# Kernel tuning notes

Measured on AMD Instinct MI355X. Metric: run time of the kernel, lower is better.

The kernel has to match this reference:

```python
import jax, jax.numpy as jnp
import numpy as np

D_MODEL = 1024
N_HEADS = 16
HEAD_DIM = D_MODEL // N_HEADS


def setup_inputs() -> dict:
    key = jax.random.key(0)
    ks = jax.random.split(key, 5)
    B, T = 4, 4096
    x = jax.random.normal(ks[0], (B, T, D_MODEL), dtype=jnp.float32)
    s = 1.0 / np.sqrt(D_MODEL)
    Wqkv = jax.random.normal(ks[1], (D_MODEL, 3 * D_MODEL), dtype=jnp.float32) * s
    bqkv = jnp.zeros((3 * D_MODEL,), dtype=jnp.float32)
    Wout = jax.random.normal(ks[2], (D_MODEL, D_MODEL), dtype=jnp.float32) * s
    bout = jnp.zeros((D_MODEL,), dtype=jnp.float32)
    return {"x": x, "Wqkv": Wqkv, "bqkv": bqkv, "Wout": Wout, "bout": bout}


def _feature_map(x):
    # elu(x) + 1  (strictly positive feature map)
    return jax.nn.elu(x) + 1.0


def reference(x, Wqkv, bqkv, Wout, bout):
    B, T, C = x.shape
    H, D = N_HEADS, HEAD_DIM
    qkv = x @ Wqkv + bqkv                      # [B,T,3C]
    qkv = qkv.reshape(B, T, 3, H, D)
    qkv = jnp.transpose(qkv, (2, 0, 3, 1, 4))  # [3,B,H,T,D]
    q, k, v = qkv[0], qkv[1], qkv[2]
    scale = D ** 0.25
    q_m = _feature_map(q / scale)
    k_m = _feature_map(k / scale)
    kv = jnp.einsum('bhtd,bhtm->bhdm', k_m, v)     # [B,H,D,D]
    out = jnp.einsum('bhtd,bhdm->bhtm', q_m, kv)   # [B,H,T,D]
    z = q_m.sum(axis=-1, keepdims=True)            # note: sum over feature dim (as in source)
    out = out / (z + 1e-6)
    out = jnp.transpose(out, (0, 2, 1, 3)).reshape(B, T, C)
    return out @ Wout + bout
```

## Files before the change

kernel.cpp:

```cpp
#include <hip/hip_runtime.h>
#include <hip/hip_bf16.h>
#include <math.h>

#define B_ 4
#define T_ 4096
#define H_ 16
#define D_ 64
#define C_ 1024
#define BT_ (B_*T_)

using short8  = __attribute__((ext_vector_type(8))) short;
using floatx4 = __attribute__((ext_vector_type(4))) float;

__device__ __forceinline__ float feature_map(float x) {
    return x > 0.0f ? x + 1.0f : __expf(x);
}
__device__ __forceinline__ unsigned short f2bf(float x) {
    union { __hip_bfloat16 b; unsigned short u; } c;
    c.b = __float2bfloat16(x);
    return c.u;
}
__device__ __forceinline__ float bf2f(unsigned short u) {
    union { unsigned int u; float f; } c;
    c.u = (unsigned)u << 16;
    return c.f;
}
__device__ __forceinline__ void async16(const void* g, void* l) {
    __builtin_amdgcn_global_load_lds(
        (const __attribute__((address_space(1))) void*)g,
        (__attribute__((address_space(3))) void*)l, 16, 0, 0);
}

__global__ __launch_bounds__(256)
void convert_x_kernel(const float4* __restrict__ x, ushort* __restrict__ xb)
{
    const size_t i = (size_t)blockIdx.x * 256 + threadIdx.x;
    const float4 v = x[i];
    *reinterpret_cast<ushort4*>(&xb[i * 4]) =
        make_ushort4(f2bf(v.x), f2bf(v.y), f2bf(v.z), f2bf(v.w));
}

__global__ __launch_bounds__(256)
void transpose_bf16_kernel(const float* __restrict__ W, ushort* __restrict__ WT,
                           int K, int N)
{
    __shared__ float t[32][33];
    const int n0 = blockIdx.x * 32, k0 = blockIdx.y * 32;
    const int r = threadIdx.x >> 5, c = threadIdx.x & 31;
    #pragma unroll
    for (int i = 0; i < 4; i++)
        t[r + 8 * i][c] = W[(size_t)(k0 + r + 8 * i) * N + n0 + c];
    __syncthreads();
    #pragma unroll
    for (int i = 0; i < 4; i++)
        WT[(size_t)(n0 + r + 8 * i) * K + k0 + c] = f2bf(t[c][r + 8 * i]);
}

__global__ __launch_bounds__(256)
void qkv_mfma_kernel(const ushort* __restrict__ xb, const ushort* __restrict__ WqkvT,
                     const float* __restrict__ bqkv,
                     ushort* __restrict__ qm, ushort* __restrict__ kmT,
                     ushort* __restrict__ vT)
{
    __shared__ __align__(16) unsigned char smem[16384];
    ushort* As = (ushort*)smem;
    ushort* Bs = (ushort*)(smem + 8192);

    const int tid = threadIdx.x;
    const int w = tid >> 6, l = tid & 63;
    const int wm = w >> 1, wn = w & 1;
    const int lr = l & 15, quad = l >> 4;
    const int lk8 = quad * 8;
    const int nBase = blockIdx.x * 128;
    const int mBase = blockIdx.y * 128;

    const int srow = w * 32 + (l >> 2);
    const int scol = (l & 3) * 8;
    const ushort* gA = xb + (size_t)(mBase + srow) * C_ + scol;
    const ushort* gB = WqkvT + (size_t)(nBase + srow) * C_ + scol;
    void* ldsA = (void*)(smem + w * 2048);
    void* ldsB = (void*)(smem + 8192 + w * 2048);

    floatx4 acc[4][4];
    #pragma unroll
    for (int i = 0; i < 4; i++)
        #pragma unroll
        for (int j = 0; j < 4; j++) acc[i][j] = (floatx4)0.0f;

    for (int k0 = 0; k0 < C_; k0 += 32) {
        __syncthreads();
        async16(gA + k0, ldsA);
        async16(gA + 16 * C_ + k0, (void*)((char*)ldsA + 1024));
        async16(gB + k0, ldsB);
        async16(gB + 16 * C_ + k0, (void*)((char*)ldsB + 1024));
        __syncthreads();

        short8 af[4], bf[4];
        #pragma unroll
        for (int mt = 0; mt < 4; mt++)
            af[mt] = *(const short8*)&As[(wm * 64 + mt * 16 + lr) * 32 + lk8];
        #pragma unroll
        for (int nt = 0; nt < 4; nt++)
            bf[nt] = *(const short8*)&Bs[(wn * 64 + nt * 16 + lr) * 32 + lk8];
        #pragma unroll
        for (int mt = 0; mt < 4; mt++)
            #pragma unroll
            for (int nt = 0; nt < 4; nt++)
                acc[mt][nt] = __builtin_amdgcn_mfma_f32_16x16x32_bf16(
                    af[mt], bf[nt], acc[mt][nt], 0, 0, 0);
    }

    const float inv_scale = 0.35355339059327373f;
    const int seg = nBase >> 10;

    if (seg == 0) {
        #pragma unroll
        for (int nt = 0; nt < 4; nt++) {
            const int c = nBase + wn * 64 + nt * 16 + lr;
            const float bv = bqkv[c];
            #pragma unroll
            for (int mt = 0; mt < 4; mt++)
                #pragma unroll
                for (int i = 0; i < 4; i++) {
                    const int t = mBase + wm * 64 + mt * 16 + quad * 4 + i;
                    qm[(size_t)t * C_ + c] =
                        f2bf(feature_map((acc[mt][nt][i] + bv) * inv_scale));
                }
        }
    } else {
        ushort* dstT = (seg == 1) ? kmT : vT;
        #pragma unroll
        for (int nt = 0; nt < 4; nt++) {
            const int cfull = nBase + wn * 64 + nt * 16 + lr;
            const int c = cfull - (seg << 10);
            const float bv = bqkv[cfull];
            #pragma unroll
            for (int mt = 0; mt < 4; mt++) {
                float v0 = acc[mt][nt][0] + bv, v1 = acc[mt][nt][1] + bv;
                float v2 = acc[mt][nt][2] + bv, v3 = acc[mt][nt][3] + bv;
                if (seg == 1) {
                    v0 = feature_map(v0 * inv_scale); v1 = feature_map(v1 * inv_scale);
                    v2 = feature_map(v2 * inv_scale); v3 = feature_map(v3 * inv_scale);
                }
                const int t = mBase + wm * 64 + mt * 16 + quad * 4;
                *(ushort4*)&dstT[(size_t)c * BT_ + t] =
                    make_ushort4(f2bf(v0), f2bf(v1), f2bf(v2), f2bf(v3));
            }
        }
    }
}

__global__ __launch_bounds__(256)
void kv_accum_kernel(const ushort* __restrict__ kmT, const ushort* __restrict__ vT,
                     float* __restrict__ kv)
{
    const int tid = threadIdx.x;
    const int w = tid >> 6, l = tid & 63;
    const int wm = w >> 1, wn = w & 1;
    const int lr = l & 15, quad = l >> 4;
    const int bh = blockIdx.y;
    const int b = bh >> 4, h = bh & 15;
    const size_t t0 = (size_t)b * T_ + (size_t)blockIdx.x * 512;

    const ushort* Ar = kmT + (size_t)(h * 64 + wm * 32 + lr) * BT_ + t0 + quad * 8;
    const ushort* Br = vT  + (size_t)(h * 64 + wn * 32 + lr) * BT_ + t0 + quad * 8;

    floatx4 acc[2][2];
    #pragma unroll
    for (int i = 0; i < 2; i++)
        #pragma unroll
        for (int j = 0; j < 2; j++) acc[i][j] = (floatx4)0.0f;

    #pragma unroll 4
    for (int tt = 0; tt < 512; tt += 32) {
        const short8 af0 = *(const short8*)&Ar[tt];
        const short8 af1 = *(const short8*)&Ar[(size_t)16 * BT_ + tt];
        const short8 bf0 = *(const short8*)&Br[tt];
        const short8 bf1 = *(const short8*)&Br[(size_t)16 * BT_ + tt];
        acc[0][0] = __builtin_amdgcn_mfma_f32_16x16x32_bf16(af0, bf0, acc[0][0], 0, 0, 0);
        acc[0][1] = __builtin_amdgcn_mfma_f32_16x16x32_bf16(af0, bf1, acc[0][1], 0, 0, 0);
        acc[1][0] = __builtin_amdgcn_mfma_f32_16x16x32_bf16(af1, bf0, acc[1][0], 0, 0, 0);
        acc[1][1] = __builtin_amdgcn_mfma_f32_16x16x32_bf16(af1, bf1, acc[1][1], 0, 0, 0);
    }

    float* kvb = kv + (size_t)bh * (D_ * D_);
    #pragma unroll
    for (int i = 0; i < 2; i++)
        #pragma unroll
        for (int j = 0; j < 2; j++)
            #pragma unroll
            for (int r = 0; r < 4; r++) {
                const int d = wm * 32 + i * 16 + quad * 4 + r;
                const int m = wn * 32 + j * 16 + lr;
                atomicAdd(&kvb[d * 64 + m], acc[i][j][r]);
            }
}

__global__ __launch_bounds__(256)
void pv_kernel(const ushort* __restrict__ qm, const float* __restrict__ kv,
               ushort* __restrict__ attn)
{
    __shared__ ushort kvs[64 * 72];
    const int tid = threadIdx.x;
    const int w = tid >> 6, l = tid & 63;
    const int lr = l & 15, quad = l >> 4;
    const int h = blockIdx.x;
    const int tBase = blockIdx.y * 256;
    const int b = tBase >> 12;

    const float* kvg = kv + ((size_t)b * H_ + h) * (D_ * D_);
    #pragma unroll
    for (int e = 0; e < 4; e++) {
        const int flat = (e * 256 + tid) * 4;
        const float4 vv = *(const float4*)&kvg[flat];
        const int d = flat >> 6, m = flat & 63;
        kvs[(m + 0) * 72 + d] = f2bf(vv.x);
        kvs[(m + 1) * 72 + d] = f2bf(vv.y);
        kvs[(m + 2) * 72 + d] = f2bf(vv.z);
        kvs[(m + 3) * 72 + d] = f2bf(vv.w);
    }
    __syncthreads();

    const int tw = tBase + w * 64;

    floatx4 acc[4][4];
    #pragma unroll
    for (int i = 0; i < 4; i++)
        #pragma unroll
        for (int j = 0; j < 4; j++) acc[i][j] = (floatx4)0.0f;

    float zp[4] = {0.0f, 0.0f, 0.0f, 0.0f};

    #pragma unroll
    for (int kk = 0; kk < 2; kk++) {
        short8 bf[4];
        #pragma unroll
        for (int tf = 0; tf < 4; tf++) {
            bf[tf] = *(const short8*)&qm[(size_t)(tw + tf * 16 + lr) * C_
                                         + h * 64 + kk * 32 + quad * 8];
            #pragma unroll
            for (int j = 0; j < 8; j++) zp[tf] += bf2f((unsigned short)bf[tf][j]);
        }
        short8 af[4];
        #pragma unroll
        for (int mf = 0; mf < 4; mf++)
            af[mf] = *(const short8*)&kvs[(mf * 16 + lr) * 72 + kk * 32 + quad * 8];
        #pragma unroll
        for (int mf = 0; mf < 4; mf++)
            #pragma unroll
            for (int tf = 0; tf < 4; tf++)
                acc[mf][tf] = __builtin_amdgcn_mfma_f32_16x16x32_bf16(
                    af[mf], bf[tf], acc[mf][tf], 0, 0, 0);
    }

    #pragma unroll
    for (int tf = 0; tf < 4; tf++) {
        zp[tf] += __shfl_xor(zp[tf], 16);
        zp[tf] += __shfl_xor(zp[tf], 32);
    }

    #pragma unroll
    for (int tf = 0; tf < 4; tf++) {
        const int t = tw + tf * 16 + lr;
        const float inv = 1.0f / (zp[tf] + 1e-6f);
        #pragma unroll
        for (int mf = 0; mf < 4; mf++) {
            const int m = mf * 16 + quad * 4;
            *(ushort4*)&attn[(size_t)t * C_ + h * 64 + m] =
                make_ushort4(f2bf(acc[mf][tf][0] * inv), f2bf(acc[mf][tf][1] * inv),
                             f2bf(acc[mf][tf][2] * inv), f2bf(acc[mf][tf][3] * inv));
        }
    }
}

__global__ __launch_bounds__(256)
void outproj_mfma_kernel(const ushort* __restrict__ attn, const ushort* __restrict__ WoutT,
                         const float* __restrict__ bout, float* __restrict__ out)
{
    __shared__ __align__(16) unsigned char smem[16384];
    ushort* As = (ushort*)smem;
    ushort* Bs = (ushort*)(smem + 8192);

    const int tid = threadIdx.x;
    const int w = tid >> 6, l = tid & 63;
    const int wm = w >> 1, wn = w & 1;
    const int lr = l & 15, lk8 = (l >> 4) * 8;
    const int mBase = blockIdx.y * 128;
    const int nBase = blockIdx.x * 128;

    const int srow = w * 32 + (l >> 2);
    const int scol = (l & 3) * 8;
    const ushort* gA = attn + (size_t)(mBase + srow) * C_ + scol;
    const ushort* gB = WoutT + (size_t)(nBase + srow) * C_ + scol;
    void* ldsA = (void*)(smem + w * 2048);
    void* ldsB = (void*)(smem + 8192 + w * 2048);

    floatx4 acc[4][4];
    #pragma unroll
    for (int i = 0; i < 4; i++)
        #pragma unroll
        for (int j = 0; j < 4; j++) acc[i][j] = (floatx4)0.0f;

    for (int k0 = 0; k0 < C_; k0 += 32) {
        __syncthreads();
        async16(gA + k0, ldsA);
        async16(gA + 16 * C_ + k0, (void*)((char*)ldsA + 1024));
        async16(gB + k0, ldsB);
        async16(gB + 16 * C_ + k0, (void*)((char*)ldsB + 1024));
        __syncthreads();

        short8 af[4], bfr[4];
        #pragma unroll
        for (int mt = 0; mt < 4; mt++)
            af[mt] = *(const short8*)&As[(wm * 64 + mt * 16 + lr) * 32 + lk8];
        #pragma unroll
        for (int nt = 0; nt < 4; nt++)
            bfr[nt] = *(const short8*)&Bs[(wn * 64 + nt * 16 + lr) * 32 + lk8];
        #pragma unroll
        for (int mt = 0; mt < 4; mt++)
            #pragma unroll
            for (int nt = 0; nt < 4; nt++)
                acc[mt][nt] = __builtin_amdgcn_mfma_f32_16x16x32_bf16(
                    af[mt], bfr[nt], acc[mt][nt], 0, 0, 0);
    }

    #pragma unroll
    for (int mt = 0; mt < 4; mt++)
        #pragma unroll
        for (int nt = 0; nt < 4; nt++) {
            const int cc = nBase + wn * 64 + nt * 16 + lr;
            const float bv = bout[cc];
            #pragma unroll
            for (int i = 0; i < 4; i++) {
                const int rr = mBase + wm * 64 + mt * 16 + (l >> 4) * 4 + i;
                out[(size_t)rr * C_ + cc] = acc[mt][nt][i] + bv;
            }
        }
}

extern "C" void kernel_launch(void* const* d_in, const int* in_sizes, int n_in,
                              void* d_out, int out_size, void* d_ws, size_t ws_size,
                              hipStream_t stream)
{
    const float* x    = (const float*)d_in[0];
    const float* Wqkv = (const float*)d_in[1];
    const float* bqkv = (const float*)d_in[2];
    const float* Wout = (const float*)d_in[3];
    const float* bout = (const float*)d_in[4];
    float* out = (float*)d_out;

    char* ws = (char*)d_ws;
    ushort* xb     = (ushort*)ws;
    ushort* WqkvT  = (ushort*)(ws + 33554432);
    ushort* WoutT  = (ushort*)(ws + 39845888);
    ushort* vT     = (ushort*)(ws + 41943040);
    float*  kv     = (float*) (ws + 75497472);
    ushort* attn   = (ushort*)ws;
    ushort* qm     = (ushort*)d_out;
    ushort* kmT    = (ushort*)((char*)d_out + 33554432);

    hipMemsetAsync(kv, 0, (size_t)B_ * H_ * D_ * D_ * sizeof(float), stream);

    convert_x_kernel<<<(BT_ * C_ / 4) / 256, 256, 0, stream>>>((const float4*)x, xb);
    transpose_bf16_kernel<<<dim3(3 * C_ / 32, C_ / 32), 256, 0, stream>>>(Wqkv, WqkvT, C_, 3 * C_);
    transpose_bf16_kernel<<<dim3(C_ / 32, C_ / 32), 256, 0, stream>>>(Wout, WoutT, C_, C_);

    qkv_mfma_kernel<<<dim3(3 * C_ / 128, BT_ / 128), 256, 0, stream>>>(
        xb, WqkvT, bqkv, qm, kmT, vT);
    kv_accum_kernel<<<dim3(8, B_ * H_), 256, 0, stream>>>(kmT, vT, kv);
    pv_kernel<<<dim3(H_, BT_ / 256), 256, 0, stream>>>(qm, kv, attn);
    outproj_mfma_kernel<<<dim3(C_ / 128, BT_ / 128), 256, 0, stream>>>(attn, WoutT, bout, out);
}
```

Baseline: 374.7 us.

## Replace QKV and out-proj GEMMs with 256x256 8-phase pipelined MFMA kernel

Both projection GEMMs now use one templated kernel with 256x256 tiles, 512 threads, and 128KB of double-buffered LDS using XOR-swizzled layout. It adds an interleaved 8-phase schedule of async global-to-LDS loads, LDS reads and MFMA bursts, with setprio and explicit waitcnt, plus an XCD-aware block remapping. The aim is to hide memory latency, raise data reuse per tile and cut the LDS bank conflicts and sync stalls of the old 128x128 single-buffer loop. The cost is heavy register pressure and fragile hand-placed synchronization. The 256-block out-proj grid may also underfill the device.

```diff
diff --git a/kernel.cpp b/kernel.cpp
--- a/kernel.cpp
+++ b/kernel.cpp
@@ -56,98 +56,190 @@
         WT[(size_t)(n0 + r + 8 * i) * K + k0 + c] = f2bf(t[c][r + 8 * i]);
 }
 
-__global__ __launch_bounds__(256)
-void qkv_mfma_kernel(const ushort* __restrict__ xb, const ushort* __restrict__ WqkvT,
-                     const float* __restrict__ bqkv,
-                     ushort* __restrict__ qm, ushort* __restrict__ kmT,
-                     ushort* __restrict__ vT)
-{
-    __shared__ __align__(16) unsigned char smem[16384];
-    ushort* As = (ushort*)smem;
-    ushort* Bs = (ushort*)(smem + 8192);
+#define BAR()    __builtin_amdgcn_s_barrier()
+#define WAITDS() do { asm volatile("s_waitcnt lgkmcnt(0)" ::: "memory"); \
+                      __builtin_amdgcn_sched_barrier(0); } while(0)
+#define VM6()    do { asm volatile("s_waitcnt vmcnt(6)" ::: "memory"); \
+                      __builtin_amdgcn_sched_barrier(0); } while(0)
+
+#define LDA(slot, mf, ks, buf) \
+    aR[slot][ks] = *(const short8*)(smem + (buf)*32768 + ((mf)>>2)*16384 + \
+                                    aRowB + ((mf)&3)*2048 + cks##ks)
+#define LDB(nf, ks, buf) \
+    bR[nf][ks] = *(const short8*)(smem + 65536 + (buf)*32768 + ((nf)>>1)*16384 + \
+                                  bRowB + ((nf)&1)*2048 + cks##ks)
+#define LDA8(MB, BUF) do { \
+    LDA(0, MB+0, 0, BUF); LDA(0, MB+0, 1, BUF); \
+    LDA(1, MB+1, 0, BUF); LDA(1, MB+1, 1, BUF); \
+    LDA(2, MB+2, 0, BUF); LDA(2, MB+2, 1, BUF); \
+    LDA(3, MB+3, 0, BUF); LDA(3, MB+3, 1, BUF); } while(0)
+#define LDB4(NF, BUF) do { \
+    LDB(NF+0, 0, BUF); LDB(NF+0, 1, BUF); \
+    LDB(NF+1, 0, BUF); LDB(NF+1, 1, BUF); } while(0)
+
+#define MM(mf, nf, ks, slot) \
+    acc[mf][nf] = __builtin_amdgcn_mfma_f32_16x16x32_bf16( \
+        aR[slot][ks], bR[nf][ks], acc[mf][nf], 0, 0, 0)
+#define MFMAQ(MB, NF) do { \
+    MM(MB+0,NF+0,0,0); MM(MB+1,NF+0,0,1); MM(MB+2,NF+0,0,2); MM(MB+3,NF+0,0,3); \
+    MM(MB+0,NF+1,0,0); MM(MB+1,NF+1,0,1); MM(MB+2,NF+1,0,2); MM(MB+3,NF+1,0,3); \
+    MM(MB+0,NF+0,1,0); MM(MB+1,NF+0,1,1); MM(MB+2,NF+0,1,2); MM(MB+3,NF+0,1,3); \
+    MM(MB+0,NF+1,1,0); MM(MB+1,NF+1,1,1); MM(MB+2,NF+1,1,2); MM(MB+3,NF+1,1,3); \
+} while(0)
+
+#define STG(SRC, OPB, h, w, buf) do { \
+    async16(SRC[h][0] + (size_t)(w)*128, \
+            smem + (OPB) + (buf)*32768 + (h)*16384 + wv*1024); \
+    async16(SRC[h][1] + (size_t)(w)*128, \
+            smem + (OPB) + (buf)*32768 + (h)*16384 + 8192 + wv*1024); \
+} while(0)
+
+template<int EPI, int NBX>
+__global__ __launch_bounds__(512, 2)
+void gemm256_8ph(const ushort* __restrict__ A, const ushort* __restrict__ Bm,
+                 const float* __restrict__ bias,
+                 ushort* __restrict__ q_out, ushort* __restrict__ kT_out,
+                 ushort* __restrict__ vT_out, float* __restrict__ f_out)
+{
+    __shared__ __align__(16) unsigned char smem[131072];
 
     const int tid = threadIdx.x;
-    const int w = tid >> 6, l = tid & 63;
-    const int wm = w >> 1, wn = w & 1;
+    const int wv = tid >> 6, l = tid & 63;
+    const int wm = wv >> 2, wn = wv & 3;
     const int lr = l & 15, quad = l >> 4;
-    const int lk8 = quad * 8;
-    const int nBase = blockIdx.x * 128;
-    const int mBase = blockIdx.y * 128;
-
-    const int srow = w * 32 + (l >> 2);
-    const int scol = (l & 3) * 8;
-    const ushort* gA = xb + (size_t)(mBase + srow) * C_ + scol;
-    const ushort* gB = WqkvT + (size_t)(nBase + srow) * C_ + scol;
-    void* ldsA = (void*)(smem + w * 2048);
-    void* ldsB = (void*)(smem + 8192 + w * 2048);
-
-    floatx4 acc[4][4];
-    #pragma unroll
-    for (int i = 0; i < 4; i++)
+
+    int wg = blockIdx.x;
+    { const int cpx = (int)gridDim.x >> 3; wg = (wg & 7) * cpx + (wg >> 3); }
+    const int mb = wg / NBX, nb = wg % NBX;
+    const int mBase = mb * 256, nBase = nb * 256;
+
+    const int s0 = tid >> 3;
+    const int cb = ((tid & 7) * 16) ^ ((s0 & 7) << 4);
+    const char* Abyte = (const char*)(A + (size_t)mBase * C_);
+    const char* Bbyte = (const char*)(Bm + (size_t)nBase * C_);
+    const char* aSrc[2][2]; const char* bSrc[2][2];
+    #pragma unroll
+    for (int h = 0; h < 2; h++) {
+        aSrc[h][0] = Abyte + (size_t)(h * 64 + s0) * 2048 + cb;
+        aSrc[h][1] = Abyte + (size_t)(128 + h * 64 + s0) * 2048 + cb;
+        const int bq = (s0 >> 5) * 64 + h * 32 + (s0 & 31);
+        bSrc[h][0] = Bbyte + (size_t)bq * 2048 + cb;
+        bSrc[h][1] = Bbyte + (size_t)(bq + 128) * 2048 + cb;
+    }
+
+    const int aRowB = (wm * 64 + lr) * 128;
+    const int bRowB = (wn * 32 + lr) * 128;
+    const int cks0 = (quad * 16) ^ ((lr & 7) << 4);
+    const int cks1 = 64 ^ cks0;
+
+    floatx4 acc[8][4];
+    #pragma unroll
+    for (int i = 0; i < 8; i++)
         #pragma unroll
         for (int j = 0; j < 4; j++) acc[i][j] = (floatx4)0.0f;
-
-    for (int k0 = 0; k0 < C_; k0 += 32) {
-        __syncthreads();
-        async16(gA + k0, ldsA);
-        async16(gA + 16 * C_ + k0, (void*)((char*)ldsA + 1024));
-        async16(gB + k0, ldsB);
-        async16(gB + 16 * C_ + k0, (void*)((char*)ldsB + 1024));
-        __syncthreads();
-
-        short8 af[4], bf[4];
-        #pragma unroll
-        for (int mt = 0; mt < 4; mt++)
-            af[mt] = *(const short8*)&As[(wm * 64 + mt * 16 + lr) * 32 + lk8];
-        #pragma unroll
-        for (int nt = 0; nt < 4; nt++)
-            bf[nt] = *(const short8*)&Bs[(wn * 64 + nt * 16 + lr) * 32 + lk8];
-        #pragma unroll
-        for (int mt = 0; mt < 4; mt++)
-            #pragma unroll
-            for (int nt = 0; nt < 4; nt++)
-                acc[mt][nt] = __builtin_amdgcn_mfma_f32_16x16x32_bf16(
-                    af[mt], bf[nt], acc[mt][nt], 0, 0, 0);
-    }
-
-    const float inv_scale = 0.35355339059327373f;
-    const int seg = nBase >> 10;
-
-    if (seg == 0) {
-        #pragma unroll
-        for (int nt = 0; nt < 4; nt++) {
-            const int c = nBase + wn * 64 + nt * 16 + lr;
-            const float bv = bqkv[c];
-            #pragma unroll
-            for (int mt = 0; mt < 4; mt++)
+    short8 aR[4][2], bR[4][2];
+
+    STG(aSrc,     0, 0, 0, 0);
+    STG(bSrc, 65536, 0, 0, 0);
+    STG(bSrc, 65536, 1, 0, 0);
+    STG(aSrc,     0, 1, 0, 0);
+    STG(aSrc,     0, 0, 1, 1);
+    STG(bSrc, 65536, 0, 1, 1);
+    STG(bSrc, 65536, 1, 1, 1);
+    asm volatile("s_waitcnt vmcnt(6)" ::: "memory");
+    __builtin_amdgcn_sched_barrier(0);
+    BAR();
+
+    #pragma unroll 1
+    for (int it = 0; it < 8; ++it) {
+        const int t1v = 2 * it + 1;
+        const int t2v = (2 * it + 2) & 15;
+        const int t3v = (2 * it + 3) & 15;
+        LDA8(0, 0); LDB4(0, 0);
+        STG(aSrc, 0, 1, t1v, 1);
+        BAR(); WAITDS(); __builtin_amdgcn_s_setprio(1); MFMAQ(0, 0);
+        __builtin_amdgcn_s_setprio(0); BAR();
+        LDB4(2, 0);
+        STG(aSrc, 0, 0, t2v, 0);
+        BAR(); WAITDS(); __builtin_amdgcn_s_setprio(1); MFMAQ(0, 2);
+        __builtin_amdgcn_s_setprio(0); BAR();
+        LDA8(4, 0);
+        STG(bSrc, 65536, 0, t2v, 0);
+        BAR(); WAITDS(); __builtin_amdgcn_s_setprio(1); MFMAQ(4, 2);
+        __builtin_amdgcn_s_setprio(0); BAR();
+        STG(bSrc, 65536, 1, t2v, 0);
+        BAR(); WAITDS(); __builtin_amdgcn_s_setprio(1); MFMAQ(4, 0);
+        __builtin_amdgcn_s_setprio(0); VM6(); BAR();
+        LDA8(0, 1); LDB4(0, 1);
+        STG(aSrc, 0, 1, t2v, 0);
+        BAR(); WAITDS(); __builtin_amdgcn_s_setprio(1); MFMAQ(0, 0);
+        __builtin_amdgcn_s_setprio(0); BAR();
+        LDB4(2, 1);
+        STG(aSrc, 0, 0, t3v, 1);
+        BAR(); WAITDS(); __builtin_amdgcn_s_setprio(1); MFMAQ(0, 2);
+        __builtin_amdgcn_s_setprio(0); BAR();
+        LDA8(4, 1);
+        STG(bSrc, 65536, 0, t3v, 1);
+        BAR(); WAITDS(); __builtin_amdgcn_s_setprio(1); MFMAQ(4, 2);
+        __builtin_amdgcn_s_setprio(0); BAR();
+        STG(bSrc, 65536, 1, t3v, 1);
+        BAR(); WAITDS(); __builtin_amdgcn_s_setprio(1); MFMAQ(4, 0);
+        __builtin_amdgcn_s_setprio(0); VM6(); BAR();
+    }
+
+    if (EPI == 0) {
+        const float inv_scale = 0.35355339059327373f;
+        const int seg = nBase >> 10;
+        if (seg == 0) {
+            #pragma unroll
+            for (int nf = 0; nf < 4; nf++) {
+                const int c = nBase + wn * 64 + nf * 16 + lr;
+                const float bv = bias[c];
+                #pragma unroll
+                for (int mf = 0; mf < 8; mf++)
+                    #pragma unroll
+                    for (int i = 0; i < 4; i++) {
+                        const int t = mBase + wm * 128 + mf * 16 + quad * 4 + i;
+                        q_out[(size_t)t * C_ + c] =
+                            f2bf(feature_map((acc[mf][nf][i] + bv) * inv_scale));
+                    }
+            }
+        } else {
+            ushort* dstT = (seg == 1) ? kT_out : vT_out;
+            #pragma unroll
+            for (int nf = 0; nf < 4; nf++) {
+                const int cfull = nBase + wn * 64 + nf * 16 + lr;
+                const int c = cfull & 1023;
+                const float bv = bias[cfull];
+                #pragma unroll
+                for (int mf = 0; mf < 8; mf++) {
+                    float v0 = acc[mf][nf][0] + bv, v1 = acc[mf][nf][1] + bv;
+                    float v2 = acc[mf][nf][2] + bv, v3 = acc[mf][nf][3] + bv;
+                    if (seg == 1) {
+                        v0 = feature_map(v0 * inv_scale); v1 = feature_map(v1 * inv_scale);
+                        v2 = feature_map(v2 * inv_scale); v3 = feature_map(v3 * inv_scale);
+                    }
+                    const int tt = mBase + wm * 128 + mf * 16 + quad * 4;
+                    *(ushort4*)&dstT[(size_t)c * BT_ + tt] =
+                        make_ushort4(f2bf(v0), f2bf(v1), f2bf(v2), f2bf(v3));
+                }
+            }
+        }
+    } else {
+        #pragma unroll
+        for (int nf = 0; nf < 4; nf++) {
+            const int c = nBase + wn * 64 + nf * 16 + lr;
+            const float bv = bias[c];
+            #pragma unroll
+            for (int mf = 0; mf < 8; mf++)
                 #pragma unroll
                 for (int i = 0; i < 4; i++) {
-                    const int t = mBase + wm * 64 + mt * 16 + quad * 4 + i;
-                    qm[(size_t)t * C_ + c] =
-                        f2bf(feature_map((acc[mt][nt][i] + bv) * inv_scale));
+                    const int row = mBase + wm * 128 + mf * 16 + quad * 4 + i;
+                    f_out[(size_t)row * C_ + c] = acc[mf][nf][i] + bv;
                 }
         }
-    } else {
-        ushort* dstT = (seg == 1) ? kmT : vT;
-        #pragma unroll
-        for (int nt = 0; nt < 4; nt++) {
-            const int cfull = nBase + wn * 64 + nt * 16 + lr;
-            const int c = cfull - (seg << 10);
-            const float bv = bqkv[cfull];
-            #pragma unroll
-            for (int mt = 0; mt < 4; mt++) {
-                float v0 = acc[mt][nt][0] + bv, v1 = acc[mt][nt][1] + bv;
-                float v2 = acc[mt][nt][2] + bv, v3 = acc[mt][nt][3] + bv;
-                if (seg == 1) {
-                    v0 = feature_map(v0 * inv_scale); v1 = feature_map(v1 * inv_scale);
-                    v2 = feature_map(v2 * inv_scale); v3 = feature_map(v3 * inv_scale);
-                }
-                const int t = mBase + wm * 64 + mt * 16 + quad * 4;
-                *(ushort4*)&dstT[(size_t)c * BT_ + t] =
-                    make_ushort4(f2bf(v0), f2bf(v1), f2bf(v2), f2bf(v3));
-            }
-        }
-    }
+    }
+    asm volatile("s_waitcnt vmcnt(0)" ::: "memory");
 }
 
 __global__ __launch_bounds__(256)
@@ -273,71 +365,6 @@
     }
 }
 
-__global__ __launch_bounds__(256)
-void outproj_mfma_kernel(const ushort* __restrict__ attn, const ushort* __restrict__ WoutT,
-                         const float* __restrict__ bout, float* __restrict__ out)
-{
-    __shared__ __align__(16) unsigned char smem[16384];
-    ushort* As = (ushort*)smem;
-    ushort* Bs = (ushort*)(smem + 8192);
-
-    const int tid = threadIdx.x;
-    const int w = tid >> 6, l = tid & 63;
-    const int wm = w >> 1, wn = w & 1;
-    const int lr = l & 15, lk8 = (l >> 4) * 8;
-    const int mBase = blockIdx.y * 128;
-    const int nBase = blockIdx.x * 128;
-
-    const int srow = w * 32 + (l >> 2);
-    const int scol = (l & 3) * 8;
-    const ushort* gA = attn + (size_t)(mBase + srow) * C_ + scol;
-    const ushort* gB = WoutT + (size_t)(nBase + srow) * C_ + scol;
-    void* ldsA = (void*)(smem + w * 2048);
-    void* ldsB = (void*)(smem + 8192 + w * 2048);
-
-    floatx4 acc[4][4];
-    #pragma unroll
-    for (int i = 0; i < 4; i++)
-        #pragma unroll
-        for (int j = 0; j < 4; j++) acc[i][j] = (floatx4)0.0f;
-
-    for (int k0 = 0; k0 < C_; k0 += 32) {
-        __syncthreads();
-        async16(gA + k0, ldsA);
-        async16(gA + 16 * C_ + k0, (void*)((char*)ldsA + 1024));
-        async16(gB + k0, ldsB);
-        async16(gB + 16 * C_ + k0, (void*)((char*)ldsB + 1024));
-        __syncthreads();
-
-        short8 af[4], bfr[4];
-        #pragma unroll
-        for (int mt = 0; mt < 4; mt++)
-            af[mt] = *(const short8*)&As[(wm * 64 + mt * 16 + lr) * 32 + lk8];
-        #pragma unroll
-        for (int nt = 0; nt < 4; nt++)
-            bfr[nt] = *(const short8*)&Bs[(wn * 64 + nt * 16 + lr) * 32 + lk8];
-        #pragma unroll
-        for (int mt = 0; mt < 4; mt++)
-            #pragma unroll
-            for (int nt = 0; nt < 4; nt++)
-                acc[mt][nt] = __builtin_amdgcn_mfma_f32_16x16x32_bf16(
-                    af[mt], bfr[nt], acc[mt][nt], 0, 0, 0);
-    }
-
-    #pragma unroll
-    for (int mt = 0; mt < 4; mt++)
-        #pragma unroll
-        for (int nt = 0; nt < 4; nt++) {
-            const int cc = nBase + wn * 64 + nt * 16 + lr;
-            const float bv = bout[cc];
-            #pragma unroll
-            for (int i = 0; i < 4; i++) {
-                const int rr = mBase + wm * 64 + mt * 16 + (l >> 4) * 4 + i;
-                out[(size_t)rr * C_ + cc] = acc[mt][nt][i] + bv;
-            }
-        }
-}
-
 extern "C" void kernel_launch(void* const* d_in, const int* in_sizes, int n_in,
                               void* d_out, int out_size, void* d_ws, size_t ws_size,
                               hipStream_t stream)
@@ -365,9 +392,10 @@
     transpose_bf16_kernel<<<dim3(3 * C_ / 32, C_ / 32), 256, 0, stream>>>(Wqkv, WqkvT, C_, 3 * C_);
     transpose_bf16_kernel<<<dim3(C_ / 32, C_ / 32), 256, 0, stream>>>(Wout, WoutT, C_, C_);
 
-    qkv_mfma_kernel<<<dim3(3 * C_ / 128, BT_ / 128), 256, 0, stream>>>(
-        xb, WqkvT, bqkv, qm, kmT, vT);
+    gemm256_8ph<0, 12><<<dim3(768), 512, 0, stream>>>(
+        xb, WqkvT, bqkv, qm, kmT, vT, nullptr);
     kv_accum_kernel<<<dim3(8, B_ * H_), 256, 0, stream>>>(kmT, vT, kv);
     pv_kernel<<<dim3(H_, BT_ / 256), 256, 0, stream>>>(qm, kv, attn);
-    outproj_mfma_kernel<<<dim3(C_ / 128, BT_ / 128), 256, 0, stream>>>(attn, WoutT, bout, out);
-}
+    gemm256_8ph<1, 4><<<dim3(256), 512, 0, stream>>>(
+        attn, WoutT, bout, nullptr, nullptr, nullptr, out);
+}
```

Result: faster. 315.2 us (-15.9%).
